# Optimization experiments

Hardware: AMD Instinct MI355X
Metric: run time of the kernel (lower is better)

The kernel has to match this reference:

```python
import jax, jax.numpy as jnp
import numpy as np

EPS = 1e-8
SEARCH = 21  # search_window_size


def _window_stack(x, S):
    """x: [B,C,Hp,Wp] (already padded). Returns [B,C,H,W,S*S] matching
    torch unfold(2,S,1).unfold(3,S,1).reshape(...,-1) ordering (h-offset major)."""
    B, C, Hp, Wp = x.shape
    H, W = Hp - S + 1, Wp - S + 1
    patches = jax.lax.conv_general_dilated_patches(
        x, filter_shape=(S, S), window_strides=(1, 1), padding='VALID',
        dimension_numbers=('NCHW', 'OIHW', 'NCHW'))  # [B, C*S*S, H, W], (C, u, v) major->minor
    patches = patches.reshape(B, C, S * S, H, W)
    return jnp.transpose(patches, (0, 1, 3, 4, 2))  # [B,C,H,W,S*S]


def setup_inputs() -> dict:
    key = jax.random.key(0)
    k1, k2 = jax.random.split(key)
    rgb = jax.random.uniform(k1, (1, 3, 256, 256), dtype=jnp.float32)  # must be in [0,1]
    h = jnp.array([0.1], dtype=jnp.float32)  # learned NLM bandwidth parameter
    return {"rgb": rgb, "h": h}


def reference(rgb, h):
    S = SEARCH
    pad = (S - 1) // 2
    # luminance (clip only affects y, not the rgb values being averaged)
    rgb_c = jnp.clip(rgb, 0.0, 1.0)
    y = 0.299 * rgb_c[:, :1] + 0.587 * rgb_c[:, 1:2] + 0.114 * rgb_c[:, 2:]  # [B,1,H,W]

    pw = ((0, 0), (0, 0), (pad, pad), (pad, pad))
    rgb_ws = _window_stack(jnp.pad(rgb, pw, mode='reflect'), S)  # [B,3,H,W,S^2]
    y_ws = _window_stack(jnp.pad(y, pw, mode='reflect'), S)      # [B,1,H,W,S^2]

    dis = (y[..., None] - y_ws) ** 2                              # [B,1,H,W,S^2]
    dis_pad = jnp.pad(dis, ((0, 0), (0, 0), (pad, pad), (pad, pad), (0, 0)), mode='reflect')
    # sum of squared diffs over an SxS spatial window per offset (matches unfold+sum)
    dis = jax.lax.reduce_window(dis_pad, 0.0, jax.lax.add,
                                (1, 1, S, S, 1), (1, 1, 1, 1, 1), 'VALID')  # [B,1,H,W,S^2]

    distances = jnp.sqrt(jax.nn.relu(dis))
    weights = jnp.exp(-distances / (jax.nn.relu(h) + EPS))        # [B,1,H,W,S^2]
    denoised = (weights * rgb_ws).sum(-1) / weights.sum(-1)       # [B,3,H,W]
    return jnp.clip(denoised, 0.0, 1.0)
```

## Files before the change

kernel.cpp:

```cpp
#include <hip/hip_runtime.h>
#include <math.h>


#define IMG 256
#define NPIX (IMG * IMG)
#define TILE 32
#define GR 52
#define YD 72
#define YSTR 78
#define HST 54
#define NOFF 441
#define NGB 8
#define NTHR 512

typedef __attribute__((ext_vector_type(4))) _Float16 half4;
typedef __attribute__((ext_vector_type(2))) _Float16 half2_t;

#if __has_builtin(__builtin_amdgcn_fdot2)
#define FDOT2(a, b, c) __builtin_amdgcn_fdot2((a), (b), (c), false)
#else
#define FDOT2(a, b, c) ((c) + (float)(a).x * (float)(b).x + (float)(a).y * (float)(b).y)
#endif

#if __has_builtin(__builtin_amdgcn_sqrtf)
#define ASQRT(x) __builtin_amdgcn_sqrtf(x)
#else
#define ASQRT(x) sqrtf(x)
#endif

__device__ __forceinline__ int refl(int t) {
    t = t < 0 ? -t : t;
    return t > 255 ? 510 - t : t;
}

template <bool DIRECT>
__global__ __launch_bounds__(NTHR, 4)
void nlm_main(const float* __restrict__ rgb, const float* __restrict__ hptr,
              float4* __restrict__ partials)
{
    __shared__ __align__(16) _Float16 Yreg[YD][YSTR];
    __shared__ __align__(16) _Float16 Creg4[GR][GR][4];
    __shared__ __align__(16) _Float16 hsT[8][TILE][HST];
    __shared__ unsigned char cjTab[21][GR];

    const int tid = threadIdx.x;
    const int tj = ((int)blockIdx.x & 7) * TILE;
    const int ti = ((int)blockIdx.x >> 3) * TILE;

    const int Ybi = min(max(ti - 20, 0), IMG - YD);
    const int Ybj = min(max(tj - 20, 0), IMG - YD);
    const bool interior = (ti >= 20) && (ti + 51 <= 255) && (tj >= 20) && (tj + 51 <= 255);

    for (int idx = tid; idx < YD * YD; idx += NTHR) {
        int a = idx / YD, b = idx - a * YD;
        int g = (Ybi + a) * IMG + (Ybj + b);
        float r  = fminf(fmaxf(rgb[g], 0.f), 1.f);
        float gg = fminf(fmaxf(rgb[NPIX + g], 0.f), 1.f);
        float bb = fminf(fmaxf(rgb[2 * NPIX + g], 0.f), 1.f);
        Yreg[a][b] = (_Float16)(0.299f * r + 0.587f * gg + 0.114f * bb);
    }
    for (int idx = tid; idx < GR * GR; idx += NTHR) {
        int t = idx / GR, b = idx - t * GR;
        int g = refl(ti - 10 + t) * IMG + refl(tj - 10 + b);
        half4 c;
        c.x = (_Float16)rgb[g];
        c.y = (_Float16)rgb[NPIX + g];
        c.z = (_Float16)rgb[2 * NPIX + g];
        c.w = (_Float16)1.f;
        *(half4*)&Creg4[t][b][0] = c;
    }
    if (!interior) {
        for (int idx = tid; idx < 21 * GR; idx += NTHR) {
            int d = idx / GR, c = idx - d * GR;
            cjTab[d][c] = (unsigned char)(refl(refl(tj - 10 + c) + (d - 10)) - Ybj);
        }
    }
    __syncthreads();

    const int lane = tid & 63;
    const int wv   = tid >> 6;
    const bool hact = lane < GR;

    half2_t y0h[26];
    if (hact) {
        if (interior) {
            const half2_t* q0 = (const half2_t*)&Yreg[lane + 10][10];
            #pragma unroll
            for (int i = 0; i < 26; ++i) y0h[i] = q0[i];
        } else {
            const _Float16* Y0row = &Yreg[refl(ti - 10 + lane) - Ybi][0];
            const unsigned char* cj0 = &cjTab[10][0];
            #pragma unroll
            for (int i = 0; i < 26; ++i) {
                half2_t v;
                v.x = Y0row[cj0[2 * i]];
                v.y = Y0row[cj0[2 * i + 1]];
                y0h[i] = v;
            }
        }
    }

    const float hv = fmaxf(hptr[0], 0.f);
    const float negI = -1.0f / (hv + 1e-8f);

    const int pb  = lane & 31;
    const int s16 = (lane >> 5) << 4;

    half2_t accRG[16], accBW[16];
    #pragma unroll
    for (int k = 0; k < 16; ++k) {
        accRG[k].x = (_Float16)0.f; accRG[k].y = (_Float16)0.f;
        accBW[k].x = (_Float16)0.f; accBW[k].y = (_Float16)0.f;
    }

    half2_t one; one.x = (_Float16)1.f; one.y = (_Float16)1.f;

    const int o0 = (int)blockIdx.y * 8 + wv;
    int du = o0 / 21 - 10;
    int dv = o0 % 21 - 10;
    for (int o = o0; o < NOFF; o += 64) {
        if (hact) {
            const int t = lane;
            half2_t ff[26];
            if (interior) {
                if ((dv & 1) == 0) {
                    const half2_t* q1 = (const half2_t*)&Yreg[t + 10 + du][10 + dv];
                    #pragma unroll
                    for (int i = 0; i < 26; ++i) {
                        half2_t d2 = y0h[i] - q1[i];
                        ff[i] = d2 * d2;
                    }
                } else {
                    const half2_t* q1 = (const half2_t*)&Yreg[t + 10 + du][10 + dv - 1];
                    half2_t prev = q1[0];
                    #pragma unroll
                    for (int i = 0; i < 26; ++i) {
                        half2_t cur = q1[i + 1];
                        half2_t b; b.x = prev.y; b.y = cur.x;
                        half2_t d2 = y0h[i] - b;
                        ff[i] = d2 * d2;
                        prev = cur;
                    }
                }
            } else {
                const unsigned int* cw = (const unsigned int*)&cjTab[dv + 10][0];
                const _Float16* Y1row = &Yreg[refl(refl(ti - 10 + t) + du) - Ybi][0];
                #pragma unroll
                for (int i = 0; i < 26; ++i) {
                    unsigned int w0 = cw[i >> 1];
                    int sh = (i & 1) * 16;
                    _Float16 a0 = Y1row[(w0 >> sh) & 0xffu];
                    _Float16 a1 = Y1row[(w0 >> (sh + 8)) & 0xffu];
                    half2_t yv; yv.x = a0; yv.y = a1;
                    half2_t d2 = y0h[i] - yv;
                    ff[i] = d2 * d2;
                }
            }
            float s0f = 0.f, s1f = 0.f;
            #pragma unroll
            for (int i = 0; i < 10; ++i) s0f = FDOT2(ff[i], one, s0f);
            s0f += (float)ff[10].x;
            #pragma unroll
            for (int i = 8; i < 18; ++i) s1f = FDOT2(ff[i], one, s1f);
            s1f += (float)ff[18].x;
            _Float16 sA = (_Float16)s0f;
            _Float16 sB = (_Float16)s1f;
            hsT[wv][0][t]  = sA;
            hsT[wv][16][t] = sB;
            #pragma unroll
            for (int k = 1; k < 16; ++k) {
                {
                    int ja = 20 + k, jb = k - 1;
                    _Float16 fa = (ja & 1) ? ff[ja >> 1].y : ff[ja >> 1].x;
                    _Float16 fb = (jb & 1) ? ff[jb >> 1].y : ff[jb >> 1].x;
                    sA += (_Float16)(fa - fb);
                    hsT[wv][k][t] = sA;
                }
                {
                    int ja = 36 + k, jb = 15 + k;
                    _Float16 fa = (ja & 1) ? ff[ja >> 1].y : ff[ja >> 1].x;
                    _Float16 fb = (jb & 1) ? ff[jb >> 1].y : ff[jb >> 1].x;
                    sB += (_Float16)(fa - fb);
                    hsT[wv][16 + k][t] = sB;
                }
            }
        }

        {
            const half2_t* col2 = (const half2_t*)&hsT[wv][pb][s16];
            half2_t w2[18];
            #pragma unroll
            for (int i = 0; i < 18; ++i) w2[i] = col2[i];

            float vs0 = 0.f, vs1 = 0.f;
            #pragma unroll
            for (int i = 0; i < 10; ++i) vs0 = FDOT2(w2[i], one, vs0);
            vs0 += (float)w2[10].x;
            #pragma unroll
            for (int i = 4; i < 14; ++i) vs1 = FDOT2(w2[i], one, vs1);
            vs1 += (float)w2[14].x;

            float vss[16];
            vss[0] = vs0;
            vss[8] = vs1;
            #pragma unroll
            for (int k = 0; k < 7; ++k) {
                {
                    int ja = 21 + k, jb = k;
                    _Float16 fa = (ja & 1) ? w2[ja >> 1].y : w2[ja >> 1].x;
                    _Float16 fb = (jb & 1) ? w2[jb >> 1].y : w2[jb >> 1].x;
                    vss[k + 1] = vss[k] + (float)(_Float16)(fa - fb);
                }
                {
                    int ja = 29 + k, jb = 8 + k;
                    _Float16 fa = (ja & 1) ? w2[ja >> 1].y : w2[ja >> 1].x;
                    _Float16 fb = (jb & 1) ? w2[jb >> 1].y : w2[jb >> 1].x;
                    vss[k + 9] = vss[k + 8] + (float)(_Float16)(fa - fb);
                }
            }

            const int cr = s16 + 10 + du;
            const int cc = pb + 10 + dv;
            #pragma unroll
            for (int k = 0; k < 16; ++k) {
                float dist = ASQRT(fmaxf(vss[k], 0.f));
                float w = __expf(dist * negI);
                _Float16 wh = (_Float16)w;
                half2_t w2v; w2v.x = wh; w2v.y = wh;
                const half2_t* cp = (const half2_t*)&Creg4[cr + k][cc][0];
                half2_t cRG = cp[0];
                half2_t cBW = cp[1];
                accRG[k] = w2v * cRG + accRG[k];
                accBW[k] = w2v * cBW + accBW[k];
            }
        }

        du += 3; dv += 1;
        if (dv > 10) { dv -= 21; du += 1; }
    }

    __syncthreads();
    float4* scratch = (float4*)&Creg4[0][0][0];
    #pragma unroll
    for (int w = 0; w < 8; ++w) {
        if (wv == w) {
            #pragma unroll
            for (int k = 0; k < 16; ++k) {
                int px = (s16 + k) * 32 + pb;
                float4 v = make_float4((float)accRG[k].x, (float)accRG[k].y,
                                       (float)accBW[k].x, (float)accBW[k].y);
                if (w == 0) scratch[px] = v;
                else {
                    float4 a = scratch[px];
                    scratch[px] = make_float4(a.x + v.x, a.y + v.y, a.z + v.z, a.w + v.w);
                }
            }
        }
        __syncthreads();
    }
    for (int i = tid; i < TILE * TILE; i += NTHR) {
        float4 v = scratch[i];
        int gpix = (ti + (i >> 5)) * IMG + (tj + (i & 31));
        if (DIRECT) {
            partials[(size_t)blockIdx.y * NPIX + gpix] = v;
        } else {
            float* p = (float*)&partials[gpix];
            atomicAdd(p + 0, v.x);
            atomicAdd(p + 1, v.y);
            atomicAdd(p + 2, v.z);
            atomicAdd(p + 3, v.w);
        }
    }
}

template <int NGT>
__global__ __launch_bounds__(256)
void nlm_finalize(const float4* __restrict__ partials, float* __restrict__ out)
{
    int idx = blockIdx.x * blockDim.x + threadIdx.x;
    float r = 0.f, g = 0.f, b = 0.f, w = 0.f;
    #pragma unroll
    for (int gg = 0; gg < NGT; ++gg) {
        float4 p = partials[(size_t)gg * NPIX + idx];
        r += p.x; g += p.y; b += p.z; w += p.w;
    }
    float inv = 1.0f / w;
    out[idx]            = fminf(fmaxf(r * inv, 0.f), 1.f);
    out[NPIX + idx]     = fminf(fmaxf(g * inv, 0.f), 1.f);
    out[2 * NPIX + idx] = fminf(fmaxf(b * inv, 0.f), 1.f);
}

extern "C" void kernel_launch(void* const* d_in, const int* in_sizes, int n_in,
                              void* d_out, int out_size, void* d_ws, size_t ws_size,
                              hipStream_t stream) {
    (void)in_sizes; (void)n_in; (void)out_size;
    const float* rgb  = (const float*)d_in[0];
    const float* hptr = (const float*)d_in[1];
    float* out = (float*)d_out;
    float4* partials = (float4*)d_ws;

    const bool direct = ws_size >= (size_t)NGB * NPIX * sizeof(float4);
    dim3 grid(64, NGB);
    if (direct) {
        nlm_main<true><<<grid, NTHR, 0, stream>>>(rgb, hptr, partials);
        nlm_finalize<NGB><<<NPIX / 256, 256, 0, stream>>>(partials, out);
    } else {
        (void)hipMemsetAsync(partials, 0, (size_t)NPIX * sizeof(float4), stream);
        nlm_main<false><<<grid, NTHR, 0, stream>>>(rgb, hptr, partials);
        nlm_finalize<1><<<NPIX / 256, 256, 0, stream>>>(partials, out);
    }
}
```

Baseline: 100.2 us.

## Software-pipeline two offsets per iteration to overlap H-phase with V-math

```diff
diff --git a/kernel.cpp b/kernel.cpp
--- a/kernel.cpp
+++ b/kernel.cpp
@@ -34,7 +34,7 @@
 }
 
 template <bool DIRECT>
-__global__ __launch_bounds__(NTHR, 4)
+__global__ __launch_bounds__(NTHR, 2)
 void nlm_main(const float* __restrict__ rgb, const float* __restrict__ hptr,
               float4* __restrict__ partials)
 {
@@ -115,128 +115,143 @@
 
     half2_t one; one.x = (_Float16)1.f; one.y = (_Float16)1.f;
 
-    const int o0 = (int)blockIdx.y * 8 + wv;
-    int du = o0 / 21 - 10;
-    int dv = o0 % 21 - 10;
-    for (int o = o0; o < NOFF; o += 64) {
-        if (hact) {
-            const int t = lane;
-            half2_t ff[26];
-            if (interior) {
-                if ((dv & 1) == 0) {
-                    const half2_t* q1 = (const half2_t*)&Yreg[t + 10 + du][10 + dv];
-                    #pragma unroll
-                    for (int i = 0; i < 26; ++i) {
-                        half2_t d2 = y0h[i] - q1[i];
-                        ff[i] = d2 * d2;
-                    }
-                } else {
-                    const half2_t* q1 = (const half2_t*)&Yreg[t + 10 + du][10 + dv - 1];
-                    half2_t prev = q1[0];
-                    #pragma unroll
-                    for (int i = 0; i < 26; ++i) {
-                        half2_t cur = q1[i + 1];
-                        half2_t b; b.x = prev.y; b.y = cur.x;
-                        half2_t d2 = y0h[i] - b;
-                        ff[i] = d2 * d2;
-                        prev = cur;
-                    }
+    auto Hphase = [&](int du, int dv) {
+        const int t = lane;
+        half2_t ff[26];
+        if (interior) {
+            if ((dv & 1) == 0) {
+                const half2_t* q1 = (const half2_t*)&Yreg[t + 10 + du][10 + dv];
+                #pragma unroll
+                for (int i = 0; i < 26; ++i) {
+                    half2_t d2 = y0h[i] - q1[i];
+                    ff[i] = d2 * d2;
                 }
             } else {
-                const unsigned int* cw = (const unsigned int*)&cjTab[dv + 10][0];
-                const _Float16* Y1row = &Yreg[refl(refl(ti - 10 + t) + du) - Ybi][0];
+                const half2_t* q1 = (const half2_t*)&Yreg[t + 10 + du][10 + dv - 1];
+                half2_t prev = q1[0];
                 #pragma unroll
                 for (int i = 0; i < 26; ++i) {
-                    unsigned int w0 = cw[i >> 1];
-                    int sh = (i & 1) * 16;
-                    _Float16 a0 = Y1row[(w0 >> sh) & 0xffu];
-                    _Float16 a1 = Y1row[(w0 >> (sh + 8)) & 0xffu];
-                    half2_t yv; yv.x = a0; yv.y = a1;
-                    half2_t d2 = y0h[i] - yv;
+                    half2_t cur = q1[i + 1];
+                    half2_t b; b.x = prev.y; b.y = cur.x;
+                    half2_t d2 = y0h[i] - b;
                     ff[i] = d2 * d2;
+                    prev = cur;
                 }
             }
-            float s0f = 0.f, s1f = 0.f;
+        } else {
+            const unsigned int* cw = (const unsigned int*)&cjTab[dv + 10][0];
+            const _Float16* Y1row = &Yreg[refl(refl(ti - 10 + t) + du) - Ybi][0];
             #pragma unroll
-            for (int i = 0; i < 10; ++i) s0f = FDOT2(ff[i], one, s0f);
-            s0f += (float)ff[10].x;
-            #pragma unroll
-            for (int i = 8; i < 18; ++i) s1f = FDOT2(ff[i], one, s1f);
-            s1f += (float)ff[18].x;
-            _Float16 sA = (_Float16)s0f;
-            _Float16 sB = (_Float16)s1f;
-            hsT[wv][0][t]  = sA;
-            hsT[wv][16][t] = sB;
-            #pragma unroll
-            for (int k = 1; k < 16; ++k) {
-                {
-                    int ja = 20 + k, jb = k - 1;
-                    _Float16 fa = (ja & 1) ? ff[ja >> 1].y : ff[ja >> 1].x;
-                    _Float16 fb = (jb & 1) ? ff[jb >> 1].y : ff[jb >> 1].x;
-                    sA += (_Float16)(fa - fb);
-                    hsT[wv][k][t] = sA;
-                }
-                {
-                    int ja = 36 + k, jb = 15 + k;
-                    _Float16 fa = (ja & 1) ? ff[ja >> 1].y : ff[ja >> 1].x;
-                    _Float16 fb = (jb & 1) ? ff[jb >> 1].y : ff[jb >> 1].x;
-                    sB += (_Float16)(fa - fb);
-                    hsT[wv][16 + k][t] = sB;
-                }
-            }
-        }
-
-        {
-            const half2_t* col2 = (const half2_t*)&hsT[wv][pb][s16];
-            half2_t w2[18];
-            #pragma unroll
-            for (int i = 0; i < 18; ++i) w2[i] = col2[i];
-
-            float vs0 = 0.f, vs1 = 0.f;
-            #pragma unroll
-            for (int i = 0; i < 10; ++i) vs0 = FDOT2(w2[i], one, vs0);
-            vs0 += (float)w2[10].x;
-            #pragma unroll
-            for (int i = 4; i < 14; ++i) vs1 = FDOT2(w2[i], one, vs1);
-            vs1 += (float)w2[14].x;
-
-            float vss[16];
-            vss[0] = vs0;
-            vss[8] = vs1;
-            #pragma unroll
-            for (int k = 0; k < 7; ++k) {
-                {
-                    int ja = 21 + k, jb = k;
-                    _Float16 fa = (ja & 1) ? w2[ja >> 1].y : w2[ja >> 1].x;
-                    _Float16 fb = (jb & 1) ? w2[jb >> 1].y : w2[jb >> 1].x;
-                    vss[k + 1] = vss[k] + (float)(_Float16)(fa - fb);
-                }
-                {
-                    int ja = 29 + k, jb = 8 + k;
-                    _Float16 fa = (ja & 1) ? w2[ja >> 1].y : w2[ja >> 1].x;
-                    _Float16 fb = (jb & 1) ? w2[jb >> 1].y : w2[jb >> 1].x;
-                    vss[k + 9] = vss[k + 8] + (float)(_Float16)(fa - fb);
-                }
-            }
-
-            const int cr = s16 + 10 + du;
-            const int cc = pb + 10 + dv;
-            #pragma unroll
-            for (int k = 0; k < 16; ++k) {
-                float dist = ASQRT(fmaxf(vss[k], 0.f));
-                float w = __expf(dist * negI);
-                _Float16 wh = (_Float16)w;
-                half2_t w2v; w2v.x = wh; w2v.y = wh;
-                const half2_t* cp = (const half2_t*)&Creg4[cr + k][cc][0];
-                half2_t cRG = cp[0];
-                half2_t cBW = cp[1];
-                accRG[k] = w2v * cRG + accRG[k];
-                accBW[k] = w2v * cBW + accBW[k];
-            }
-        }
-
-        du += 3; dv += 1;
-        if (dv > 10) { dv -= 21; du += 1; }
+            for (int i = 0; i < 26; ++i) {
+                unsigned int w0 = cw[i >> 1];
+                int sh = (i & 1) * 16;
+                _Float16 a0 = Y1row[(w0 >> sh) & 0xffu];
+                _Float16 a1 = Y1row[(w0 >> (sh + 8)) & 0xffu];
+                half2_t yv; yv.x = a0; yv.y = a1;
+                half2_t d2 = y0h[i] - yv;
+                ff[i] = d2 * d2;
+            }
+        }
+        float s0f = 0.f, s1f = 0.f;
+        #pragma unroll
+        for (int i = 0; i < 10; ++i) s0f = FDOT2(ff[i], one, s0f);
+        s0f += (float)ff[10].x;
+        #pragma unroll
+        for (int i = 8; i < 18; ++i) s1f = FDOT2(ff[i], one, s1f);
+        s1f += (float)ff[18].x;
+        _Float16 sA = (_Float16)s0f;
+        _Float16 sB = (_Float16)s1f;
+        hsT[wv][0][t]  = sA;
+        hsT[wv][16][t] = sB;
+        #pragma unroll
+        for (int k = 1; k < 16; ++k) {
+            {
+                int ja = 20 + k, jb = k - 1;
+                _Float16 fa = (ja & 1) ? ff[ja >> 1].y : ff[ja >> 1].x;
+                _Float16 fb = (jb & 1) ? ff[jb >> 1].y : ff[jb >> 1].x;
+                sA += (_Float16)(fa - fb);
+                hsT[wv][k][t] = sA;
+            }
+            {
+                int ja = 36 + k, jb = 15 + k;
+                _Float16 fa = (ja & 1) ? ff[ja >> 1].y : ff[ja >> 1].x;
+                _Float16 fb = (jb & 1) ? ff[jb >> 1].y : ff[jb >> 1].x;
+                sB += (_Float16)(fa - fb);
+                hsT[wv][16 + k][t] = sB;
+            }
+        }
+    };
+
+    auto Vread = [&](half2_t (&w2)[18]) {
+        const half2_t* col2 = (const half2_t*)&hsT[wv][pb][s16];
+        #pragma unroll
+        for (int i = 0; i < 18; ++i) w2[i] = col2[i];
+    };
+
+    auto Vmath = [&](int du, int dv, half2_t (&w2)[18]) {
+        float vs0 = 0.f, vs1 = 0.f;
+        #pragma unroll
+        for (int i = 0; i < 10; ++i) vs0 = FDOT2(w2[i], one, vs0);
+        vs0 += (float)w2[10].x;
+        #pragma unroll
+        for (int i = 4; i < 14; ++i) vs1 = FDOT2(w2[i], one, vs1);
+        vs1 += (float)w2[14].x;
+
+        float vss[16];
+        vss[0] = vs0;
+        vss[8] = vs1;
+        #pragma unroll
+        for (int k = 0; k < 7; ++k) {
+            {
+                int ja = 21 + k, jb = k;
+                _Float16 fa = (ja & 1) ? w2[ja >> 1].y : w2[ja >> 1].x;
+                _Float16 fb = (jb & 1) ? w2[jb >> 1].y : w2[jb >> 1].x;
+                vss[k + 1] = vss[k] + (float)(_Float16)(fa - fb);
+            }
+            {
+                int ja = 29 + k, jb = 8 + k;
+                _Float16 fa = (ja & 1) ? w2[ja >> 1].y : w2[ja >> 1].x;
+                _Float16 fb = (jb & 1) ? w2[jb >> 1].y : w2[jb >> 1].x;
+                vss[k + 9] = vss[k + 8] + (float)(_Float16)(fa - fb);
+            }
+        }
+
+        const int cr = s16 + 10 + du;
+        const int cc = pb + 10 + dv;
+        #pragma unroll
+        for (int k = 0; k < 16; ++k) {
+            float dist = ASQRT(fmaxf(vss[k], 0.f));
+            float w = __expf(dist * negI);
+            _Float16 wh = (_Float16)w;
+            half2_t w2v; w2v.x = wh; w2v.y = wh;
+            const half2_t* cp = (const half2_t*)&Creg4[cr + k][cc][0];
+            half2_t cRG = cp[0];
+            half2_t cBW = cp[1];
+            accRG[k] = w2v * cRG + accRG[k];
+            accBW[k] = w2v * cBW + accBW[k];
+        }
+    };
+
+    const int o0 = (int)blockIdx.y * 8 + wv;
+    int duA = o0 / 21 - 10,       dvA = o0 % 21 - 10;
+    int duB = (o0 + 64) / 21 - 10, dvB = (o0 + 64) % 21 - 10;
+    half2_t w2A[18], w2B[18];
+
+    #pragma unroll 1
+    for (int m = 0; m < 3; ++m) {
+        if (hact) Hphase(duA, dvA);
+        Vread(w2A);
+        if (hact) Hphase(duB, dvB);
+        Vmath(duA, dvA, w2A);
+        Vread(w2B);
+        Vmath(duB, dvB, w2B);
+        duA += 6; dvA += 2; if (dvA > 10) { dvA -= 21; duA += 1; }
+        duB += 6; dvB += 2; if (dvB > 10) { dvB -= 21; duB += 1; }
+    }
+    if (o0 + 384 < NOFF) {
+        if (hact) Hphase(duA, dvA);
+        Vread(w2A);
+        Vmath(duA, dvA, w2A);
     }
 
     __syncthreads();
```

After: 99.42 us. About the same (-0.8%).
